# Optimization experiments

Measured on AMD Instinct MI355X. Metric: run time of the kernel, lower is better.

## Reference

```python
import jax, jax.numpy as jnp
import numpy as np

EMBED_DIM = 1024
NHEAD = 16
HEAD_DIM = EMBED_DIM // NHEAD  # 64
B, S = 2, 2048


def _rotate_half(x):
    x1, x2 = jnp.split(x, 2, axis=-1)
    return jnp.concatenate([-x2, x1], axis=-1)


def _apply_rope(t, cos, sin):
    # t: (B, H, S, Dh); cos/sin: (S, Dh) broadcast over leading dims
    return t * cos + _rotate_half(t) * sin


def setup_inputs() -> dict:
    key = jax.random.key(0)
    ks = jax.random.split(key, 6)
    x = jax.random.normal(ks[0], (B, S, EMBED_DIM), dtype=jnp.float32)
    # real RoPE tables: theta_i = 10000^(-2i/Dh), duplicated for the two halves
    inv_freq = 1.0 / (10000.0 ** (jnp.arange(0, HEAD_DIM, 2, dtype=jnp.float32) / HEAD_DIM))
    freqs = jnp.outer(jnp.arange(S, dtype=jnp.float32), inv_freq)  # (S, Dh/2)
    emb = jnp.concatenate([freqs, freqs], axis=-1)  # (S, Dh)
    cos = jnp.cos(emb)
    sin = jnp.sin(emb)
    W_in = jax.random.normal(ks[1], (EMBED_DIM, 3 * EMBED_DIM), dtype=jnp.float32) * 0.02
    b_in = jax.random.normal(ks[2], (3 * EMBED_DIM,), dtype=jnp.float32) * 0.02
    W_out = jax.random.normal(ks[3], (EMBED_DIM, EMBED_DIM), dtype=jnp.float32) * 0.02
    b_out = jax.random.normal(ks[4], (EMBED_DIM,), dtype=jnp.float32) * 0.02
    return {"x": x, "cos": cos, "sin": sin, "W_in": W_in, "b_in": b_in,
            "W_out": W_out, "b_out": b_out}


def reference(x, cos, sin, W_in, b_in, W_out, b_out):
    Bs, Ss, D = x.shape
    qkv = x @ W_in + b_in  # (B, S, 3D)
    q, k, v = jnp.split(qkv, 3, axis=-1)
    # (B, S, D) -> (B, H, S, Dh)
    def heads(t):
        return t.reshape(Bs, Ss, NHEAD, HEAD_DIM).transpose(0, 2, 1, 3)
    q, k, v = heads(q), heads(k), heads(v)
    q = _apply_rope(q, cos, sin)
    k = _apply_rope(k, cos, sin)
    scale = 1.0 / jnp.sqrt(jnp.array(HEAD_DIM, dtype=x.dtype))
    scores = jnp.einsum('bhqd,bhkd->bhqk', q, k) * scale
    attn = jax.nn.softmax(scores, axis=-1)
    out = jnp.einsum('bhqk,bhkd->bhqd', attn, v)
    out = out.transpose(0, 2, 1, 3).reshape(Bs, Ss, D)
    return out @ W_out + b_out
```

## Files before the change

### kernel.cpp

```cpp
#include <hip/hip_runtime.h>
#include <hip/hip_bf16.h>

typedef float f32x4 __attribute__((ext_vector_type(4)));
typedef float f32x16 __attribute__((ext_vector_type(16)));
typedef short s16x8 __attribute__((ext_vector_type(8)));

typedef const __attribute__((address_space(1))) unsigned int* as1u;
typedef __attribute__((address_space(3))) unsigned int* as3u;

__device__ __forceinline__ unsigned short f2bf(float f) {
    union { float f; unsigned u; } v; v.f = f;
    unsigned u = v.u;
    u += 0x7fffu + ((u >> 16) & 1u);
    return (unsigned short)(u >> 16);
}

__device__ __forceinline__ void gload16(const void* g, void* l3) {
    __builtin_amdgcn_global_load_lds((as1u)g, (as3u)l3, 16, 0, 0);
}

__device__ __forceinline__ int swzo(int row, int cb) {
    return row * 128 + (cb ^ ((row & 7) << 4));
}

#define LOG2E 1.4426950408889634f
#define QSCALE (0.125f * LOG2E)

__global__ __launch_bounds__(256) void prep_kernel(
    const float* __restrict__ x, unsigned short* __restrict__ xb,
    const float* __restrict__ W_in, unsigned short* __restrict__ Wt_in,
    const float* __restrict__ W_out, unsigned short* __restrict__ Wot)
{
    const int t = threadIdx.x;
    int blk = blockIdx.x;
    if (blk < 2048) {
        size_t i = ((size_t)blk * 256 + t) * 8;
        float4 a = *(const float4*)&x[i];
        float4 b = *(const float4*)&x[i + 4];
        s16x8 p;
        p[0] = (short)f2bf(a.x); p[1] = (short)f2bf(a.y);
        p[2] = (short)f2bf(a.z); p[3] = (short)f2bf(a.w);
        p[4] = (short)f2bf(b.x); p[5] = (short)f2bf(b.y);
        p[6] = (short)f2bf(b.z); p[7] = (short)f2bf(b.w);
        *(s16x8*)&xb[i] = p;
        return;
    }
    const float* W;
    unsigned short* Wt;
    int N;
    if (blk < 2816) { blk -= 2048; W = W_in;  Wt = Wt_in; N = 3072; }
    else            { blk -= 2816; W = W_out; Wt = Wot;   N = 1024; }
    __shared__ alignas(16) short T[64 * 64];
    const int KB = 16;
    const int kb = blk % KB, nb = blk / KB;
#pragma unroll
    for (int pass = 0; pass < 4; ++pass) {
        int k = pass * 16 + (t >> 4);
        int n4 = (t & 15) * 4;
        float4 v = *(const float4*)&W[(size_t)(kb * 64 + k) * N + nb * 64 + n4];
        short4 s4;
        s4.x = (short)f2bf(v.x); s4.y = (short)f2bf(v.y);
        s4.z = (short)f2bf(v.z); s4.w = (short)f2bf(v.w);
        *(short4*)((char*)T + k * 128 + ((n4 * 2) ^ ((k & 7) << 4))) = s4;
    }
    __syncthreads();
#pragma unroll
    for (int pass = 0; pass < 4; ++pass) {
        int n = pass * 16 + (t >> 4);
        int k4 = (t & 15) * 4;
        short4 s4;
        s4.x = *(const short*)((const char*)T + (k4 + 0) * 128 + ((n * 2) ^ (((k4 + 0) & 7) << 4)));
        s4.y = *(const short*)((const char*)T + (k4 + 1) * 128 + ((n * 2) ^ (((k4 + 1) & 7) << 4)));
        s4.z = *(const short*)((const char*)T + (k4 + 2) * 128 + ((n * 2) ^ (((k4 + 2) & 7) << 4)));
        s4.w = *(const short*)((const char*)T + (k4 + 3) * 128 + ((n * 2) ^ (((k4 + 3) & 7) << 4)));
        *(short4*)&Wt[(size_t)(nb * 64 + n) * 1024 + kb * 64 + k4] = s4;
    }
}

__global__ __launch_bounds__(512, 2) void qkv_rope_kernel(
    const unsigned short* __restrict__ xb, const unsigned short* __restrict__ Wt,
    const float* __restrict__ bias, const float* __restrict__ cosb,
    const float* __restrict__ sinb,
    unsigned short* __restrict__ Qb, unsigned short* __restrict__ Kb,
    unsigned short* __restrict__ Vb)
{
    __shared__ alignas(16) short As[2][256 * 64];
    __shared__ alignas(16) short Bs[2][256 * 64];
    const int bid = blockIdx.x;
    const int mb = bid & 15, nb = bid >> 4;
    const int t = threadIdx.x, w = t >> 6, l = t & 63;
    const int g = l >> 4, j = l & 15;
    const int wm = w >> 2, wn = w & 3;
    const int m0 = mb * 256, n0 = nb * 256;

    f32x4 acc[8][4];
#pragma unroll
    for (int mi = 0; mi < 8; ++mi)
#pragma unroll
        for (int ni = 0; ni < 4; ++ni) acc[mi][ni] = (f32x4){0.f, 0.f, 0.f, 0.f};

#pragma unroll
    for (int i = 0; i < 4; ++i) {
        int p = (w * 4 + i) * 1024 + l * 16;
        int r = p >> 7, lb = (p & 127) ^ ((r & 7) << 4);
        gload16(&xb[(size_t)(m0 + r) * 1024 + (lb >> 1)], (char*)As[0] + (w * 4 + i) * 1024);
        gload16(&Wt[(size_t)(n0 + r) * 1024 + (lb >> 1)], (char*)Bs[0] + (w * 4 + i) * 1024);
    }
    asm volatile("s_waitcnt vmcnt(0)" ::: "memory");
    __builtin_amdgcn_s_barrier();

    for (int kti = 0; kti < 16; ++kti) {
        const int cur = kti & 1, nxt = cur ^ 1;
        const int ktn = ((kti + 1) & 15) * 64;

#pragma unroll
        for (int i = 0; i < 4; ++i) {
            int p = (w * 4 + i) * 1024 + l * 16;
            int r = p >> 7, lb = (p & 127) ^ ((r & 7) << 4);
            gload16(&xb[(size_t)(m0 + r) * 1024 + ktn + (lb >> 1)], (char*)As[nxt] + (w * 4 + i) * 1024);
            gload16(&Wt[(size_t)(n0 + r) * 1024 + ktn + (lb >> 1)], (char*)Bs[nxt] + (w * 4 + i) * 1024);
        }
        asm volatile("s_waitcnt vmcnt(8)" ::: "memory");
        __builtin_amdgcn_s_barrier();

#pragma unroll
        for (int kf = 0; kf < 2; ++kf) {
            s16x8 bv[4];
#pragma unroll
            for (int ni = 0; ni < 4; ++ni)
                bv[ni] = *(const s16x8*)((const char*)Bs[cur] + swzo(wn * 64 + ni * 16 + j, kf * 64 + g * 16));
#pragma unroll
            for (int mh = 0; mh < 2; ++mh) {
                s16x8 af[4];
#pragma unroll
                for (int mi = 0; mi < 4; ++mi)
                    af[mi] = *(const s16x8*)((const char*)As[cur] + swzo(wm * 128 + mh * 64 + mi * 16 + j, kf * 64 + g * 16));
                __builtin_amdgcn_s_setprio(1);
#pragma unroll
                for (int mi = 0; mi < 4; ++mi)
#pragma unroll
                    for (int ni = 0; ni < 4; ++ni)
                        acc[mh * 4 + mi][ni] = __builtin_amdgcn_mfma_f32_16x16x32_bf16(af[mi], bv[ni], acc[mh * 4 + mi][ni], 0, 0, 0);
                __builtin_amdgcn_s_setprio(0);
            }
        }
        __builtin_amdgcn_s_barrier();
    }

    const int row0 = m0 + wm * 128;
    const int col0 = n0 + wn * 64;
    const int sec = col0 >> 10;
    const int h = (col0 & 1023) >> 6;

    if (sec < 2) {
        unsigned short* dst = (sec == 0) ? Qb : Kb;
        const float qs = (sec == 0) ? QSCALE : 1.0f;
#pragma unroll
        for (int nt = 0; nt < 2; ++nt) {
            const int d = nt * 16 + j;
            const float b1 = bias[col0 + d];
            const float b2 = bias[col0 + d + 32];
#pragma unroll
            for (int mi = 0; mi < 8; ++mi) {
#pragma unroll
                for (int r = 0; r < 4; ++r) {
                    int row = row0 + mi * 16 + g * 4 + r;
                    int s = row & 2047, bb = row >> 11;
                    float c = cosb[s * 64 + d], sn = sinb[s * 64 + d];
                    float x1 = acc[mi][nt][r] + b1;
                    float x2 = acc[mi][nt + 2][r] + b2;
                    float lo = (x1 * c - x2 * sn) * qs;
                    float hi = (x1 * sn + x2 * c) * qs;
                    size_t base = ((size_t)(bb * 16 + h) * 2048 + s) * 64;
                    dst[base + d] = f2bf(lo);
                    dst[base + d + 32] = f2bf(hi);
                }
            }
        }
    } else {
#pragma unroll
        for (int nt = 0; nt < 4; ++nt) {
            const int d = nt * 16 + j;
            const float bvv = bias[col0 + d];
#pragma unroll
            for (int mi = 0; mi < 8; ++mi) {
#pragma unroll
                for (int r = 0; r < 4; ++r) {
                    int row = row0 + mi * 16 + g * 4 + r;
                    int s = row & 2047, bb = row >> 11;
                    size_t base = ((size_t)(bb * 16 + h) * 2048 + s) * 64;
                    Vb[base + d] = f2bf(acc[mi][nt][r] + bvv);
                }
            }
        }
    }
}

#define NROUND 16
__global__ __launch_bounds__(512) void attn_kernel(
    const unsigned short* __restrict__ Qb, const unsigned short* __restrict__ Kb,
    const unsigned short* __restrict__ Vb, unsigned short* __restrict__ AO)
{
    __shared__ alignas(16) short Ks[2][2 * 64 * 64];
    __shared__ alignas(16) short Vt[2][2 * 64 * 64];
    const int bid = blockIdx.x;
    const int xcd = bid & 7, idx = bid >> 3;
    const int bh = xcd + 8 * (idx & 3);
    const int qt = idx >> 2;
    const int t = threadIdx.x, w = t >> 6, l = t & 63;
    const int lq = l & 31, lh = l >> 5;
    const unsigned short* Qh = Qb + (size_t)bh * 131072;
    const unsigned short* Kh = Kb + (size_t)bh * 131072;
    const unsigned short* Vh = Vb + (size_t)bh * 131072;
    const int q0 = qt * 256 + w * 32;

    s16x8 aq[4];
#pragma unroll
    for (int ds = 0; ds < 4; ++ds)
        aq[ds] = *(const s16x8*)&Qh[(size_t)(q0 + lq) * 64 + ds * 16 + lh * 8];

    float lt_ = 0.f;
    f32x16 o[2];
#pragma unroll
    for (int i = 0; i < 16; ++i) { o[0][i] = 0.f; o[1][i] = 0.f; }

    const bool vrole = (w < 4);
    const int tv = t & 255;
    const int vk = (tv & 31) * 2;
    const int vd = (tv >> 5) * 8;
    const int kw = (w & 3);

    s16x8 va[2], vb2[2];

    if (vrole) {
#pragma unroll
        for (int s = 0; s < 2; ++s) {
            va[s]  = *(const s16x8*)&Vh[(size_t)(s * 64 + vk) * 64 + vd];
            vb2[s] = *(const s16x8*)&Vh[(size_t)(s * 64 + vk + 1) * 64 + vd];
        }
    } else {
#pragma unroll
        for (int i = 0; i < 4; ++i) {
            int p = (kw * 4 + i) * 1024 + l * 16;
            int s = p >> 13, q = p & 8191;
            int r = q >> 7, lb = (q & 127) ^ ((r & 7) << 4);
            gload16(&Kh[(size_t)(s * 64 + r) * 64 + (lb >> 1)],
                    (char*)Ks[0] + (kw * 4 + i) * 1024);
        }
    }
    asm volatile("s_waitcnt vmcnt(0)" ::: "memory");
    if (vrole) {
#pragma unroll
        for (int s = 0; s < 2; ++s)
#pragma unroll
            for (int dd = 0; dd < 8; ++dd) {
                int d = vd + dd;
                unsigned pkv = (unsigned)(unsigned short)va[s][dd] | ((unsigned)(unsigned short)vb2[s][dd] << 16);
                *(unsigned*)((char*)Vt[0] + s * 8192 + d * 128 + ((vk * 2) ^ ((d & 7) << 4))) = pkv;
            }
    }
    asm volatile("s_waitcnt lgkmcnt(0)" ::: "memory");
    __builtin_amdgcn_s_barrier();

    for (int rr = 0; rr < NROUND; ++rr) {
        const int cur = rr & 1, nxt = cur ^ 1;
        const int kvp = ((rr + 1) & (NROUND - 1)) * 128;

        if (vrole) {
#pragma unroll
            for (int s = 0; s < 2; ++s) {
                va[s]  = *(const s16x8*)&Vh[(size_t)(kvp + s * 64 + vk) * 64 + vd];
                vb2[s] = *(const s16x8*)&Vh[(size_t)(kvp + s * 64 + vk + 1) * 64 + vd];
            }
        } else {
#pragma unroll
            for (int i = 0; i < 4; ++i) {
                int p = (kw * 4 + i) * 1024 + l * 16;
                int s = p >> 13, q = p & 8191;
                int r = q >> 7, lb = (q & 127) ^ ((r & 7) << 4);
                gload16(&Kh[(size_t)(kvp + s * 64 + r) * 64 + (lb >> 1)],
                        (char*)Ks[nxt] + (kw * 4 + i) * 1024);
            }
        }

#pragma unroll
        for (int sub = 0; sub < 2; ++sub) {
            const char* kbase = (const char*)Ks[cur] + sub * 8192;
            const char* vbase = (const char*)Vt[cur] + sub * 8192;

            f32x16 sc[2];
#pragma unroll
            for (int i = 0; i < 16; ++i) { sc[0][i] = 0.f; sc[1][i] = 0.f; }
            __builtin_amdgcn_s_setprio(1);
#pragma unroll
            for (int kh = 0; kh < 2; ++kh)
#pragma unroll
                for (int ds = 0; ds < 4; ++ds) {
                    s16x8 kf = *(const s16x8*)(kbase + swzo(kh * 32 + lq, ds * 32 + lh * 16));
                    sc[kh] = __builtin_amdgcn_mfma_f32_32x32x16_bf16(kf, aq[ds], sc[kh], 0, 0, 0);
                }
            __builtin_amdgcn_s_setprio(0);

            float rs = 0.f;
#pragma unroll
            for (int kh = 0; kh < 2; ++kh)
#pragma unroll
                for (int r = 0; r < 16; ++r) {
                    sc[kh][r] = __builtin_amdgcn_exp2f(sc[kh][r]);
                    rs += sc[kh][r];
                }
            lt_ += rs;

#pragma unroll
            for (int kh = 0; kh < 2; ++kh) {
                unsigned X[8];
#pragma unroll
                for (int i = 0; i < 8; ++i)
                    asm("v_cvt_pk_bf16_f32 %0, %1, %2"
                        : "=v"(X[i]) : "v"(sc[kh][2 * i]), "v"(sc[kh][2 * i + 1]));
#pragma unroll
                for (int ks = 0; ks < 2; ++ks) {
                    unsigned a0 = X[ks * 4 + 0], a1 = X[ks * 4 + 1];
                    unsigned b0 = X[ks * 4 + 2], b1 = X[ks * 4 + 3];
                    asm("v_permlane32_swap_b32 %0, %1" : "+v"(a0), "+v"(b0));
                    asm("v_permlane32_swap_b32 %0, %1" : "+v"(a1), "+v"(b1));
                    union { unsigned u[4]; s16x8 v; } fr;
                    fr.u[0] = a0; fr.u[1] = a1; fr.u[2] = b0; fr.u[3] = b1;
                    const int kst = kh * 2 + ks;
                    __builtin_amdgcn_s_setprio(1);
#pragma unroll
                    for (int dh = 0; dh < 2; ++dh) {
                        s16x8 vf = *(const s16x8*)(vbase + swzo(dh * 32 + lq, kst * 32 + lh * 16));
                        o[dh] = __builtin_amdgcn_mfma_f32_32x32x16_bf16(fr.v, vf, o[dh], 0, 0, 0);
                    }
                    __builtin_amdgcn_s_setprio(0);
                }
            }
        }

        if (vrole) {
#pragma unroll
            for (int s = 0; s < 2; ++s)
#pragma unroll
                for (int dd = 0; dd < 8; ++dd) {
                    int d = vd + dd;
                    unsigned pkv = (unsigned)(unsigned short)va[s][dd] | ((unsigned)(unsigned short)vb2[s][dd] << 16);
                    *(unsigned*)((char*)Vt[nxt] + s * 8192 + d * 128 + ((vk * 2) ^ ((d & 7) << 4))) = pkv;
                }
        }
        asm volatile("s_waitcnt vmcnt(0) lgkmcnt(0)" ::: "memory");
        __builtin_amdgcn_s_barrier();
    }

    lt_ += __shfl_xor(lt_, 32);
    float inv = 1.0f / lt_;

    const int b = bh >> 4, h = bh & 15;
#pragma unroll
    for (int r = 0; r < 16; ++r) {
        int qrow = (r & 3) + 8 * (r >> 2) + 4 * lh;
        float iv = __shfl(inv, qrow | (l & 32));
        int s = q0 + qrow;
        size_t base = ((size_t)b * 2048 + s) * 1024 + h * 64;
#pragma unroll
        for (int dh = 0; dh < 2; ++dh)
            AO[base + dh * 32 + lq] = f2bf(o[dh][r] * iv);
    }
}

__global__ __launch_bounds__(256, 2) void out_gemm_kernel(
    const unsigned short* __restrict__ A, const unsigned short* __restrict__ Wot,
    const float* __restrict__ bias, float* __restrict__ out)
{
    __shared__ alignas(16) short As[2][128 * 64];
    __shared__ alignas(16) short Bs[2][128 * 64];
    const int bid = blockIdx.x;
    const int xcd = bid & 7, ii = bid >> 3;
    const int mb = (xcd & 3) * 8 + (ii & 7);
    const int nb = (xcd >> 2) * 4 + (ii >> 3);
    const int t = threadIdx.x, w = t >> 6, l = t & 63;
    const int g = l >> 4, j = l & 15;
    const int wm = w >> 1, wn = w & 1;
    const int m0 = mb * 128, n0 = nb * 128;

    f32x4 acc[4][4];
#pragma unroll
    for (int mi = 0; mi < 4; ++mi)
#pragma unroll
        for (int ni = 0; ni < 4; ++ni) acc[mi][ni] = (f32x4){0.f, 0.f, 0.f, 0.f};

#pragma unroll
    for (int i = 0; i < 4; ++i) {
        int p = (w * 4 + i) * 1024 + l * 16;
        int r = p >> 7, lb = (p & 127) ^ ((r & 7) << 4);
        gload16(&A[(size_t)(m0 + r) * 1024 + (lb >> 1)], (char*)As[0] + (w * 4 + i) * 1024);
        gload16(&Wot[(size_t)(n0 + r) * 1024 + (lb >> 1)], (char*)Bs[0] + (w * 4 + i) * 1024);
    }
    asm volatile("s_waitcnt vmcnt(0)" ::: "memory");
    __builtin_amdgcn_s_barrier();

    for (int kti = 0; kti < 16; ++kti) {
        const int cur = kti & 1, nxt = cur ^ 1;
        const int ktn = ((kti + 1) & 15) * 64;

#pragma unroll
        for (int i = 0; i < 4; ++i) {
            int p = (w * 4 + i) * 1024 + l * 16;
            int r = p >> 7, lb = (p & 127) ^ ((r & 7) << 4);
            gload16(&A[(size_t)(m0 + r) * 1024 + ktn + (lb >> 1)], (char*)As[nxt] + (w * 4 + i) * 1024);
            gload16(&Wot[(size_t)(n0 + r) * 1024 + ktn + (lb >> 1)], (char*)Bs[nxt] + (w * 4 + i) * 1024);
        }
        asm volatile("s_waitcnt vmcnt(8)" ::: "memory");
        __builtin_amdgcn_s_barrier();

#pragma unroll
        for (int kf = 0; kf < 2; ++kf) {
            s16x8 af[4], bv[4];
#pragma unroll
            for (int mi = 0; mi < 4; ++mi)
                af[mi] = *(const s16x8*)((const char*)As[cur] + swzo(wm * 64 + mi * 16 + j, kf * 64 + g * 16));
#pragma unroll
            for (int ni = 0; ni < 4; ++ni)
                bv[ni] = *(const s16x8*)((const char*)Bs[cur] + swzo(wn * 64 + ni * 16 + j, kf * 64 + g * 16));
            __builtin_amdgcn_s_setprio(1);
#pragma unroll
            for (int mi = 0; mi < 4; ++mi)
#pragma unroll
                for (int ni = 0; ni < 4; ++ni)
                    acc[mi][ni] = __builtin_amdgcn_mfma_f32_16x16x32_bf16(af[mi], bv[ni], acc[mi][ni], 0, 0, 0);
            __builtin_amdgcn_s_setprio(0);
        }
        __builtin_amdgcn_s_barrier();
    }

    const int row0 = m0 + wm * 64;
    const int col0 = n0 + wn * 64;
#pragma unroll
    for (int ni = 0; ni < 4; ++ni) {
        const int col = col0 + ni * 16 + j;
        const float bvv = bias[col];
#pragma unroll
        for (int mi = 0; mi < 4; ++mi)
#pragma unroll
            for (int r = 0; r < 4; ++r) {
                int row = row0 + mi * 16 + g * 4 + r;
                out[(size_t)row * 1024 + col] = acc[mi][ni][r] + bvv;
            }
    }
}

extern "C" void kernel_launch(void* const* d_in, const int* in_sizes, int n_in,
                              void* d_out, int out_size, void* d_ws, size_t ws_size,
                              hipStream_t stream) {
    const float* x     = (const float*)d_in[0];
    const float* cosb  = (const float*)d_in[1];
    const float* sinb  = (const float*)d_in[2];
    const float* W_in  = (const float*)d_in[3];
    const float* b_in  = (const float*)d_in[4];
    const float* W_out = (const float*)d_in[5];
    const float* b_out = (const float*)d_in[6];
    float* out = (float*)d_out;

    const size_t HBUF = 2ull * 16 * 2048 * 64;
    if (ws_size < (4 * HBUF + 1024 * 1024) * sizeof(unsigned short)) return;
    unsigned short* Qb = (unsigned short*)d_ws;
    unsigned short* Kb = Qb + HBUF;
    unsigned short* Vb = Kb + HBUF;
    unsigned short* R  = Vb + HBUF;
    unsigned short* Wt_in = R;
    unsigned short* AO    = R;
    unsigned short* Wot   = R + HBUF;
    unsigned short* xbuf  = (unsigned short*)d_out;

    hipLaunchKernelGGL(prep_kernel, dim3(3072), dim3(256), 0, stream,
                       x, xbuf, W_in, Wt_in, W_out, Wot);
    hipLaunchKernelGGL(qkv_rope_kernel, dim3(192), dim3(512), 0, stream,
                       xbuf, Wt_in, b_in, cosb, sinb, Qb, Kb, Vb);
    hipLaunchKernelGGL(attn_kernel, dim3(256), dim3(512), 0, stream,
                       Qb, Kb, Vb, AO);
    hipLaunchKernelGGL(out_gemm_kernel, dim3(256), dim3(256), 0, stream,
                       AO, Wot, b_out, out);
}
```

Before: 121.5 us.

## Restructure attention into smaller 4-wave blocks with 64-key tiles and uniform roles

The attention kernel moves from 256 blocks of 8 waves (128-query tiles per wave group, 128-key rounds, split K/V loader roles) to 512 blocks of 4 waves, each block covering 128 queries and iterating over 64-key tiles. Every wave now loads part of both K (via LDS direct loads) and V (transposed through registers), and LDS per block is halved. The aim is more resident blocks per CU and better latency hiding on the 256-CU device. The trade-off is twice as many barriers and K/V reloads per query, since each block covers fewer queries.

```diff
diff --git a/kernel.cpp b/kernel.cpp
--- a/kernel.cpp
+++ b/kernel.cpp
@@ -196,23 +196,22 @@
     }
 }
 
-#define NROUND 16
-__global__ __launch_bounds__(512) void attn_kernel(
+#define NT64 32
+__global__ __launch_bounds__(256, 4) void attn_kernel(
     const unsigned short* __restrict__ Qb, const unsigned short* __restrict__ Kb,
     const unsigned short* __restrict__ Vb, unsigned short* __restrict__ AO)
 {
-    __shared__ alignas(16) short Ks[2][2 * 64 * 64];
-    __shared__ alignas(16) short Vt[2][2 * 64 * 64];
+    __shared__ alignas(16) short Ks[2][64 * 64];
+    __shared__ alignas(16) short Vt[2][64 * 64];
     const int bid = blockIdx.x;
-    const int xcd = bid & 7, idx = bid >> 3;
-    const int bh = xcd + 8 * (idx & 3);
-    const int qt = idx >> 2;
+    const int bh = (bid & 7) + ((bid >> 7) << 3);
+    const int qt = (bid >> 3) & 15;
     const int t = threadIdx.x, w = t >> 6, l = t & 63;
     const int lq = l & 31, lh = l >> 5;
     const unsigned short* Qh = Qb + (size_t)bh * 131072;
     const unsigned short* Kh = Kb + (size_t)bh * 131072;
     const unsigned short* Vh = Vb + (size_t)bh * 131072;
-    const int q0 = qt * 256 + w * 32;
+    const int q0 = qt * 128 + w * 32;
 
     s16x8 aq[4];
 #pragma unroll
@@ -224,129 +223,98 @@
 #pragma unroll
     for (int i = 0; i < 16; ++i) { o[0][i] = 0.f; o[1][i] = 0.f; }
 
-    const bool vrole = (w < 4);
-    const int tv = t & 255;
-    const int vk = (tv & 31) * 2;
-    const int vd = (tv >> 5) * 8;
-    const int kw = (w & 3);
-
-    s16x8 va[2], vb2[2];
-
-    if (vrole) {
-#pragma unroll
-        for (int s = 0; s < 2; ++s) {
-            va[s]  = *(const s16x8*)&Vh[(size_t)(s * 64 + vk) * 64 + vd];
-            vb2[s] = *(const s16x8*)&Vh[(size_t)(s * 64 + vk + 1) * 64 + vd];
-        }
-    } else {
-#pragma unroll
-        for (int i = 0; i < 4; ++i) {
-            int p = (kw * 4 + i) * 1024 + l * 16;
-            int s = p >> 13, q = p & 8191;
-            int r = q >> 7, lb = (q & 127) ^ ((r & 7) << 4);
-            gload16(&Kh[(size_t)(s * 64 + r) * 64 + (lb >> 1)],
-                    (char*)Ks[0] + (kw * 4 + i) * 1024);
-        }
+    const int vk = (t & 31) * 2;
+    const int vd = (t >> 5) * 8;
+
+    s16x8 va, vb2;
+
+    va  = *(const s16x8*)&Vh[(size_t)vk * 64 + vd];
+    vb2 = *(const s16x8*)&Vh[(size_t)(vk + 1) * 64 + vd];
+#pragma unroll
+    for (int i = 0; i < 2; ++i) {
+        int p = (w * 2 + i) * 1024 + l * 16;
+        int r = p >> 7, lb = (p & 127) ^ ((r & 7) << 4);
+        gload16(&Kh[(size_t)r * 64 + (lb >> 1)], (char*)Ks[0] + (w * 2 + i) * 1024);
     }
     asm volatile("s_waitcnt vmcnt(0)" ::: "memory");
-    if (vrole) {
-#pragma unroll
-        for (int s = 0; s < 2; ++s)
-#pragma unroll
-            for (int dd = 0; dd < 8; ++dd) {
-                int d = vd + dd;
-                unsigned pkv = (unsigned)(unsigned short)va[s][dd] | ((unsigned)(unsigned short)vb2[s][dd] << 16);
-                *(unsigned*)((char*)Vt[0] + s * 8192 + d * 128 + ((vk * 2) ^ ((d & 7) << 4))) = pkv;
-            }
+#pragma unroll
+    for (int dd = 0; dd < 8; ++dd) {
+        int d = vd + dd;
+        unsigned pkv = (unsigned)(unsigned short)va[dd] | ((unsigned)(unsigned short)vb2[dd] << 16);
+        *(unsigned*)((char*)Vt[0] + d * 128 + ((vk * 2) ^ ((d & 7) << 4))) = pkv;
     }
     asm volatile("s_waitcnt lgkmcnt(0)" ::: "memory");
     __builtin_amdgcn_s_barrier();
 
-    for (int rr = 0; rr < NROUND; ++rr) {
-        const int cur = rr & 1, nxt = cur ^ 1;
-        const int kvp = ((rr + 1) & (NROUND - 1)) * 128;
-
-        if (vrole) {
-#pragma unroll
-            for (int s = 0; s < 2; ++s) {
-                va[s]  = *(const s16x8*)&Vh[(size_t)(kvp + s * 64 + vk) * 64 + vd];
-                vb2[s] = *(const s16x8*)&Vh[(size_t)(kvp + s * 64 + vk + 1) * 64 + vd];
-            }
-        } else {
-#pragma unroll
-            for (int i = 0; i < 4; ++i) {
-                int p = (kw * 4 + i) * 1024 + l * 16;
-                int s = p >> 13, q = p & 8191;
-                int r = q >> 7, lb = (q & 127) ^ ((r & 7) << 4);
-                gload16(&Kh[(size_t)(kvp + s * 64 + r) * 64 + (lb >> 1)],
-                        (char*)Ks[nxt] + (kw * 4 + i) * 1024);
-            }
-        }
-
-#pragma unroll
-        for (int sub = 0; sub < 2; ++sub) {
-            const char* kbase = (const char*)Ks[cur] + sub * 8192;
-            const char* vbase = (const char*)Vt[cur] + sub * 8192;
-
-            f32x16 sc[2];
-#pragma unroll
-            for (int i = 0; i < 16; ++i) { sc[0][i] = 0.f; sc[1][i] = 0.f; }
-            __builtin_amdgcn_s_setprio(1);
-#pragma unroll
-            for (int kh = 0; kh < 2; ++kh)
-#pragma unroll
-                for (int ds = 0; ds < 4; ++ds) {
-                    s16x8 kf = *(const s16x8*)(kbase + swzo(kh * 32 + lq, ds * 32 + lh * 16));
-                    sc[kh] = __builtin_amdgcn_mfma_f32_32x32x16_bf16(kf, aq[ds], sc[kh], 0, 0, 0);
+    for (int tt = 0; tt < NT64; ++tt) {
+        const int cur = tt & 1, nxt = cur ^ 1;
+        const int kvp = ((tt + 1) & (NT64 - 1)) * 64;
+
+        va  = *(const s16x8*)&Vh[(size_t)(kvp + vk) * 64 + vd];
+        vb2 = *(const s16x8*)&Vh[(size_t)(kvp + vk + 1) * 64 + vd];
+#pragma unroll
+        for (int i = 0; i < 2; ++i) {
+            int p = (w * 2 + i) * 1024 + l * 16;
+            int r = p >> 7, lb = (p & 127) ^ ((r & 7) << 4);
+            gload16(&Kh[(size_t)(kvp + r) * 64 + (lb >> 1)], (char*)Ks[nxt] + (w * 2 + i) * 1024);
+        }
+
+        const char* kbase = (const char*)Ks[cur];
+        const char* vbase = (const char*)Vt[cur];
+        f32x16 sc[2];
+#pragma unroll
+        for (int i = 0; i < 16; ++i) { sc[0][i] = 0.f; sc[1][i] = 0.f; }
+        __builtin_amdgcn_s_setprio(1);
+#pragma unroll
+        for (int kh = 0; kh < 2; ++kh)
+#pragma unroll
+            for (int ds = 0; ds < 4; ++ds) {
+                s16x8 kf = *(const s16x8*)(kbase + swzo(kh * 32 + lq, ds * 32 + lh * 16));
+                sc[kh] = __builtin_amdgcn_mfma_f32_32x32x16_bf16(kf, aq[ds], sc[kh], 0, 0, 0);
+            }
+        __builtin_amdgcn_s_setprio(0);
+
+        float rs = 0.f;
+#pragma unroll
+        for (int kh = 0; kh < 2; ++kh)
+#pragma unroll
+            for (int r = 0; r < 16; ++r) {
+                sc[kh][r] = __builtin_amdgcn_exp2f(sc[kh][r]);
+                rs += sc[kh][r];
+            }
+        lt_ += rs;
+
+#pragma unroll
+        for (int kh = 0; kh < 2; ++kh) {
+            unsigned X[8];
+#pragma unroll
+            for (int i = 0; i < 8; ++i)
+                asm("v_cvt_pk_bf16_f32 %0, %1, %2"
+                    : "=v"(X[i]) : "v"(sc[kh][2 * i]), "v"(sc[kh][2 * i + 1]));
+#pragma unroll
+            for (int ks = 0; ks < 2; ++ks) {
+                unsigned a0 = X[ks * 4 + 0], a1 = X[ks * 4 + 1];
+                unsigned b0 = X[ks * 4 + 2], b1 = X[ks * 4 + 3];
+                asm("v_permlane32_swap_b32 %0, %1" : "+v"(a0), "+v"(b0));
+                asm("v_permlane32_swap_b32 %0, %1" : "+v"(a1), "+v"(b1));
+                union { unsigned u[4]; s16x8 v; } fr;
+                fr.u[0] = a0; fr.u[1] = a1; fr.u[2] = b0; fr.u[3] = b1;
+                const int kst = kh * 2 + ks;
+                __builtin_amdgcn_s_setprio(1);
+#pragma unroll
+                for (int dh = 0; dh < 2; ++dh) {
+                    s16x8 vf = *(const s16x8*)(vbase + swzo(dh * 32 + lq, kst * 32 + lh * 16));
+                    o[dh] = __builtin_amdgcn_mfma_f32_32x32x16_bf16(fr.v, vf, o[dh], 0, 0, 0);
                 }
-            __builtin_amdgcn_s_setprio(0);
-
-            float rs = 0.f;
-#pragma unroll
-            for (int kh = 0; kh < 2; ++kh)
-#pragma unroll
-                for (int r = 0; r < 16; ++r) {
-                    sc[kh][r] = __builtin_amdgcn_exp2f(sc[kh][r]);
-                    rs += sc[kh][r];
-                }
-            lt_ += rs;
-
-#pragma unroll
-            for (int kh = 0; kh < 2; ++kh) {
-                unsigned X[8];
-#pragma unroll
-                for (int i = 0; i < 8; ++i)
-                    asm("v_cvt_pk_bf16_f32 %0, %1, %2"
-                        : "=v"(X[i]) : "v"(sc[kh][2 * i]), "v"(sc[kh][2 * i + 1]));
-#pragma unroll
-                for (int ks = 0; ks < 2; ++ks) {
-                    unsigned a0 = X[ks * 4 + 0], a1 = X[ks * 4 + 1];
-                    unsigned b0 = X[ks * 4 + 2], b1 = X[ks * 4 + 3];
-                    asm("v_permlane32_swap_b32 %0, %1" : "+v"(a0), "+v"(b0));
-                    asm("v_permlane32_swap_b32 %0, %1" : "+v"(a1), "+v"(b1));
-                    union { unsigned u[4]; s16x8 v; } fr;
-                    fr.u[0] = a0; fr.u[1] = a1; fr.u[2] = b0; fr.u[3] = b1;
-                    const int kst = kh * 2 + ks;
-                    __builtin_amdgcn_s_setprio(1);
-#pragma unroll
-                    for (int dh = 0; dh < 2; ++dh) {
-                        s16x8 vf = *(const s16x8*)(vbase + swzo(dh * 32 + lq, kst * 32 + lh * 16));
-                        o[dh] = __builtin_amdgcn_mfma_f32_32x32x16_bf16(fr.v, vf, o[dh], 0, 0, 0);
-                    }
-                    __builtin_amdgcn_s_setprio(0);
-                }
-            }
-        }
-
-        if (vrole) {
-#pragma unroll
-            for (int s = 0; s < 2; ++s)
-#pragma unroll
-                for (int dd = 0; dd < 8; ++dd) {
-                    int d = vd + dd;
-                    unsigned pkv = (unsigned)(unsigned short)va[s][dd] | ((unsigned)(unsigned short)vb2[s][dd] << 16);
-                    *(unsigned*)((char*)Vt[nxt] + s * 8192 + d * 128 + ((vk * 2) ^ ((d & 7) << 4))) = pkv;
-                }
+                __builtin_amdgcn_s_setprio(0);
+            }
+        }
+
+#pragma unroll
+        for (int dd = 0; dd < 8; ++dd) {
+            int d = vd + dd;
+            unsigned pkv = (unsigned)(unsigned short)va[dd] | ((unsigned)(unsigned short)vb2[dd] << 16);
+            *(unsigned*)((char*)Vt[nxt] + d * 128 + ((vk * 2) ^ ((d & 7) << 4))) = pkv;
         }
         asm volatile("s_waitcnt vmcnt(0) lgkmcnt(0)" ::: "memory");
         __builtin_amdgcn_s_barrier();
@@ -476,7 +444,7 @@
                        x, xbuf, W_in, Wt_in, W_out, Wot);
     hipLaunchKernelGGL(qkv_rope_kernel, dim3(192), dim3(512), 0, stream,
                        xbuf, Wt_in, b_in, cosb, sinb, Qb, Kb, Vb);
-    hipLaunchKernelGGL(attn_kernel, dim3(256), dim3(512), 0, stream,
+    hipLaunchKernelGGL(attn_kernel, dim3(512), dim3(256), 0, stream,
                        Qb, Kb, Vb, AO);
     hipLaunchKernelGGL(out_gemm_kernel, dim3(256), dim3(256), 0, stream,
                        AO, Wot, b_out, out);
```

Result: slower. 125.3 us (+3.1%).
